# Kernel optimization log

Hardware: AMD Instinct MI355X
Metric: run time of the kernel (lower is better)

The kernel has to match this reference:

```python
import jax, jax.numpy as jnp
import numpy as np

B, L, IN_DIM, D, H, NCONV = 64, 400, 500, 128, 8, 4
HD = D // H  # head dim = 16


def _conv1d(x, w, b, pad, groups=1):
    # x: [B, L, Cin], w: [k, Cin//groups, Cout]
    y = jax.lax.conv_general_dilated(
        x, w, window_strides=(1,), padding=[(pad, pad)],
        dimension_numbers=('NWC', 'WIO', 'NWC'), feature_group_count=groups)
    return y + b


def _layernorm(x, g, b, eps=1e-5):
    mu = jnp.mean(x, axis=-1, keepdims=True)
    var = jnp.mean(jnp.square(x - mu), axis=-1, keepdims=True)
    return (x - mu) * jax.lax.rsqrt(var + eps) * g + b


def _posenc(L, d):
    pos = jnp.arange(L, dtype=jnp.float32)[:, None]                 # [L,1]
    div = jnp.exp(jnp.arange(0, d, 2, dtype=jnp.float32) * (-jnp.log(10000.0) / d))
    ang = pos * div                                                 # [L, d/2]
    return jnp.stack([jnp.sin(ang), jnp.cos(ang)], axis=-1).reshape(L, d)


def setup_inputs() -> dict:
    key = jax.random.key(0)
    ks = jax.random.split(key, 24)
    s = lambda k, shape, scale: jax.random.normal(k, shape, dtype=jnp.float32) * scale
    inp = {
        'x': s(ks[0], (B, L, IN_DIM), 1.0),
        # init conv: k=5, 500 -> 128
        'w_init': s(ks[1], (5, IN_DIM, D), 0.02),
        'b_init': jnp.zeros((D,), jnp.float32),
        # 4 depthwise-separable conv layers (pre-LN, residual): depthwise k=7
        'ln_conv_g': jnp.ones((NCONV, D), jnp.float32),
        'ln_conv_b': jnp.zeros((NCONV, D), jnp.float32),
        'w_dw': s(ks[2], (NCONV, 7, 1, D), 0.1),
        'b_dw': jnp.zeros((NCONV, D), jnp.float32),
        'w_pw': s(ks[3], (NCONV, 1, D, D), 0.05),
        'b_pw': jnp.zeros((NCONV, D), jnp.float32),
        # self-attention (pre-LN, residual)
        'ln_att_g': jnp.ones((D,), jnp.float32),
        'ln_att_b': jnp.zeros((D,), jnp.float32),
        'wq': s(ks[4], (D, D), 0.05), 'bq': jnp.zeros((D,), jnp.float32),
        'wk': s(ks[5], (D, D), 0.05), 'bk': jnp.zeros((D,), jnp.float32),
        'wv': s(ks[6], (D, D), 0.05), 'bv': jnp.zeros((D,), jnp.float32),
        'wo': s(ks[7], (D, D), 0.05), 'bo': jnp.zeros((D,), jnp.float32),
        # FFN (pre-LN, residual)
        'ln_ffn_g': jnp.ones((D,), jnp.float32),
        'ln_ffn_b': jnp.zeros((D,), jnp.float32),
        'w1': s(ks[8], (D, D), 0.05), 'b1': jnp.zeros((D,), jnp.float32),
        'w2': s(ks[9], (D, D), 0.05), 'b2': jnp.zeros((D,), jnp.float32),
    }
    return inp


def reference(x, w_init, b_init, ln_conv_g, ln_conv_b, w_dw, b_dw, w_pw, b_pw,
              ln_att_g, ln_att_b, wq, bq, wk, bk, wv, bv, wo, bo,
              ln_ffn_g, ln_ffn_b, w1, b1, w2, b2):
    # 1) init conv (Conv1d k=5 pad=2, 500 -> 128); torch permutes, equivalent NWC conv
    h = _conv1d(x, w_init, b_init, pad=2)                    # [B, L, D]
    # 2) positional encoding
    h = h + _posenc(h.shape[1], D)
    for i in range(NCONV):
        res = h
        h = _layernorm(h, ln_conv_g[i], ln_conv_b[i])
        h = _conv1d(h, w_dw[i], b_dw[i], pad=3, groups=D)    # depthwise k=7
        h = _conv1d(h, w_pw[i], b_pw[i], pad=0)              # pointwise 1x1
        h = jax.nn.relu(h) + res
    # 4) multi-head self-attention, pre-LN + residual
    res = h
    hn = _layernorm(h, ln_att_g, ln_att_b)
    q = (hn @ wq + bq).reshape(B, L, H, HD)
    k = (hn @ wk + bk).reshape(B, L, H, HD)
    v = (hn @ wv + bv).reshape(B, L, H, HD)
    scores = jnp.einsum('bqhd,bkhd->bhqk', q, k) / jnp.sqrt(jnp.float32(HD))
    attn = jax.nn.softmax(scores, axis=-1)
    o = jnp.einsum('bhqk,bkhd->bqhd', attn, v).reshape(B, L, D)
    h = o @ wo + bo + res
    # 5) FFN, pre-LN + residual
    res = h
    hn = _layernorm(h, ln_ffn_g, ln_ffn_b)
    h = jax.nn.relu(hn @ w1 + b1) @ w2 + b2 + res
    return h
```

## Files before the change

kernel.cpp:

```cpp
#include <hip/hip_runtime.h>
#include <hip/hip_bf16.h>
#include <math.h>

#define B 64
#define L 400
#define IN_DIM 500
#define D 128
#define H 8
#define HD 16
#define NCONV 4
#define BL (B*L)

typedef __attribute__((ext_vector_type(8))) unsigned short ushort8;
typedef __attribute__((ext_vector_type(8))) short bf16x8;
typedef __attribute__((ext_vector_type(4))) float f32x4;

__device__ __forceinline__ unsigned short f2bf(float f) {
    unsigned u = __float_as_uint(f);
    unsigned r = (u + 0x7fffu + ((u >> 16) & 1u)) >> 16;
    return (unsigned short)r;
}
__device__ __forceinline__ float bf2f(unsigned short u) {
    return __uint_as_float(((unsigned)u) << 16);
}
__device__ __forceinline__ unsigned cvtpk_bf16(float lo, float hi) {
    unsigned r;
    asm("v_cvt_pk_bf16_f32 %0, %1, %2" : "=v"(r) : "v"(lo), "v"(hi));
    return r;
}

__device__ __forceinline__ void gload16(const void* g, void* l) {
    __builtin_amdgcn_global_load_lds(
        (const __attribute__((address_space(1))) unsigned int*)g,
        (__attribute__((address_space(3))) unsigned int*)l,
        16, 0, 0);
}

__global__ __launch_bounds__(256) void k_cvt_all(
        const float* __restrict__ x, unsigned short* __restrict__ xb,
        const float* __restrict__ w_init, unsigned short* __restrict__ wbt,
        const float* __restrict__ w_pw, const float* __restrict__ wq,
        const float* __restrict__ wk, const float* __restrict__ wv,
        const float* __restrict__ wo, const float* __restrict__ w1,
        const float* __restrict__ w2, unsigned short* __restrict__ wt) {
    int bid = blockIdx.x;
    if (bid < 6464) {
        int idx = bid * 256 + threadIdx.x;
        int row = idx >> 6, ch = idx & 63;
        int b = row / 404, rr = row - b * 404;
        ushort8 o = (ushort8)0;
        if (rr >= 2 && rr < 402) {
            int l = rr - 2;
            const float* src = x + ((size_t)b * 400 + l) * 500 + ch * 8;
            if (ch < 62) {
                float4 v0 = *(const float4*)(src);
                float4 v1 = *(const float4*)(src + 4);
                o[0] = f2bf(v0.x); o[1] = f2bf(v0.y); o[2] = f2bf(v0.z); o[3] = f2bf(v0.w);
                o[4] = f2bf(v1.x); o[5] = f2bf(v1.y); o[6] = f2bf(v1.z); o[7] = f2bf(v1.w);
            } else {
#pragma unroll
                for (int j = 0; j < 8; ++j) {
                    int c = ch * 8 + j;
                    o[j] = (c < 500) ? f2bf(src[j]) : (unsigned short)0;
                }
            }
        }
        *(ushort8*)(xb + (size_t)idx * 8) = o;
    } else if (bid < 7744) {
        int idx = (bid - 6464) * 256 + threadIdx.x;
        int k = idx & 511, n = (idx >> 9) & 127, t = idx >> 16;
        float v = (k < 500) ? w_init[((size_t)t * 500 + k) * 128 + n] : 0.f;
        wbt[idx] = f2bf(v);
    } else {
        int rb = bid - 7744;
        const float* arr[10] = {w_pw, w_pw + 16384, w_pw + 2 * 16384,
                                w_pw + 3 * 16384, wq, wk, wv, wo, w1, w2};
        int widx = rb >> 6;
        const float* w = arr[widx];
        int idx = ((rb & 63) << 8) + threadIdx.x;
        int n = idx >> 7, k = idx & 127;
        wt[(size_t)widx * 16384 + idx] = f2bf(w[k * 128 + n]);
    }
}

#define TM 80
#define BK 64
__global__ __launch_bounds__(256) void k_initconv_mfma(
        const unsigned short* __restrict__ xb,
        const unsigned short* __restrict__ wbt,
        const float* __restrict__ bias, float* __restrict__ out) {
    __shared__ unsigned short As[84 * BK];
    __shared__ unsigned short Ws[5][64 * BK];
    int tid = threadIdx.x;
    int b = blockIdx.x / 10;
    int rem = blockIdx.x - b * 10;
    int l0 = (rem >> 1) * TM;
    int nh = rem & 1;
    int lane = tid & 63, wave = tid >> 6;
    int kgrp = lane >> 4, lm = lane & 15;

    f32x4 acc[5];
#pragma unroll
    for (int mf = 0; mf < 5; ++mf) acc[mf] = (f32x4)0.f;

    const unsigned short* abase = xb + ((size_t)(b * 404 + l0)) * 512;
    const unsigned short* wbase = wbt + (size_t)nh * 64 * 512;

    for (int k0 = 0; k0 < 512; k0 += BK) {
        for (int idx = tid; idx < 672; idx += 256) {
            int r = idx >> 3, sc = idx & 7;
            gload16(abase + (size_t)r * 512 + k0 + ((sc ^ (r & 7)) * 8),
                    As + idx * 8);
        }
#pragma unroll
        for (int i = 0; i < 10; ++i) {
            int idx = tid + i * 256;
            int t = idx >> 9;
            int sub = idx & 511;
            int n = sub >> 3, sc = sub & 7;
            gload16(wbase + (size_t)t * 128 * 512 + (size_t)n * 512 + k0
                        + ((sc ^ (n & 7)) * 8),
                    &Ws[t][0] + sub * 8);
        }
        __syncthreads();
        int n16 = wave * 16 + lm;
#pragma unroll
        for (int ks = 0; ks < 2; ++ks) {
            int gc = ks * 4 + kgrp;
            bf16x8 bfr[5];
#pragma unroll
            for (int t = 0; t < 5; ++t)
                bfr[t] = *(const bf16x8*)(&Ws[t][0] + n16 * 64
                                          + ((gc ^ (n16 & 7)) * 8));
#pragma unroll
            for (int mf = 0; mf < 5; ++mf) {
#pragma unroll
                for (int t = 0; t < 5; ++t) {
                    int r = mf * 16 + lm + t;
                    bf16x8 af = *(const bf16x8*)(As + r * 64
                                                 + ((gc ^ (r & 7)) * 8));
                    acc[mf] = __builtin_amdgcn_mfma_f32_16x16x32_bf16(
                        af, bfr[t], acc[mf], 0, 0, 0);
                }
            }
        }
        __syncthreads();
    }

    {
        int n = nh * 64 + wave * 16 + lm;
        float bs = bias[n];
        float pbase = expf(-(float)(n & ~1) * (9.210340371976184f / 128.0f));
#pragma unroll
        for (int mf = 0; mf < 5; ++mf) {
#pragma unroll
            for (int r = 0; r < 4; ++r) {
                int l = l0 + mf * 16 + kgrp * 4 + r;
                float ang = (float)l * pbase;
                float pe = (n & 1) ? cosf(ang) : sinf(ang);
                out[((size_t)b * 400 + l) * 128 + n] = acc[mf][r] + bs + pe;
            }
        }
    }
}

#define CB_ROWS 38
__global__ __launch_bounds__(256) void k_convblock(
        const float* __restrict__ hin, float* __restrict__ hout,
        const float* __restrict__ lng, const float* __restrict__ lnb,
        const float* __restrict__ wdw, const float* __restrict__ bdw,
        const unsigned short* __restrict__ wpt, const float* __restrict__ bpw) {
    __shared__ unsigned short Ws[128 * 128];
    __shared__ unsigned short Ln[CB_ROWS * 128];
    __shared__ unsigned short Dw[32 * 128];
    int tid = threadIdx.x;
    int b = blockIdx.x / 13;
    int tile = blockIdx.x - b * 13;
    int l0 = tile * 32;
    int lv = (l0 + 32 <= L) ? 32 : (L - l0);
    int lane = tid & 63, wave = tid >> 6;
    int lm = lane & 15, kgrp = lane >> 4;

#pragma unroll
    for (int i = 0; i < 8; ++i) {
        int idx = tid + i * 256;
        int n = idx >> 4, sc = idx & 15;
        gload16(wpt + (size_t)n * 128 + ((sc ^ (n & 15)) * 8), Ws + idx * 8);
    }

    {
        float2 gg = *(const float2*)(lng + lane * 2);
        float2 bb = *(const float2*)(lnb + lane * 2);
#pragma unroll
        for (int ri = 0; ri < 10; ++ri) {
            int r = wave + ri * 4;
            if (r < CB_ROWS) {
                int gl = l0 - 3 + r;
                bool ok = (gl >= 0 && gl < L);
                float2 v = make_float2(0.f, 0.f);
                if (ok) v = *(const float2*)(hin + ((size_t)b * L + gl) * 128 + lane * 2);
                float s = v.x + v.y;
                float q = v.x * v.x + v.y * v.y;
#pragma unroll
                for (int off = 32; off; off >>= 1) {
                    s += __shfl_xor(s, off);
                    q += __shfl_xor(q, off);
                }
                float mu  = s * (1.f / 128.f);
                float var = q * (1.f / 128.f) - mu * mu;
                float inv = rsqrtf(var + 1e-5f);
                unsigned pk = 0;
                if (ok) {
                    float ox = (v.x - mu) * inv * gg.x + bb.x;
                    float oy = (v.y - mu) * inv * gg.y + bb.y;
                    pk = (unsigned)f2bf(ox) | ((unsigned)f2bf(oy) << 16);
                }
                *(unsigned*)(Ln + r * 128 + lane * 2) = pk;
            }
        }
    }
    __syncthreads();

    {
        int d = tid & 127, half = tid >> 7;
        float wr[7];
#pragma unroll
        for (int t = 0; t < 7; ++t) wr[t] = wdw[t * 128 + d];
        float bs = bdw[d];
        float win[7];
#pragma unroll
        for (int t = 0; t < 6; ++t) win[t] = bf2f(Ln[(half * 16 + t) * 128 + d]);
#pragma unroll
        for (int lj = 0; lj < 16; ++lj) {
            int l = half * 16 + lj;
            win[6] = bf2f(Ln[(l + 6) * 128 + d]);
            float a = bs;
#pragma unroll
            for (int t = 0; t < 7; ++t) a = fmaf(win[t], wr[t], a);
#pragma unroll
            for (int t = 0; t < 6; ++t) win[t] = win[t + 1];
            Dw[l * 128 + ((d >> 3) ^ (l & 15)) * 8 + (d & 7)] = f2bf(a);
        }
    }
    __syncthreads();

    f32x4 acc[2][2];
#pragma unroll
    for (int mf = 0; mf < 2; ++mf)
#pragma unroll
        for (int nt = 0; nt < 2; ++nt) acc[mf][nt] = (f32x4)0.f;
#pragma unroll
    for (int kc = 0; kc < 4; ++kc) {
        int c = kc * 4 + kgrp;
        bf16x8 af[2];
#pragma unroll
        for (int mf = 0; mf < 2; ++mf) {
            int r = mf * 16 + lm;
            af[mf] = *(const bf16x8*)(Dw + r * 128 + (c ^ (r & 15)) * 8);
        }
#pragma unroll
        for (int nt = 0; nt < 2; ++nt) {
            int n = wave * 32 + nt * 16 + lm;
            bf16x8 bfv = *(const bf16x8*)(Ws + n * 128 + (c ^ (n & 15)) * 8);
#pragma unroll
            for (int mf = 0; mf < 2; ++mf)
                acc[mf][nt] = __builtin_amdgcn_mfma_f32_16x16x32_bf16(
                    af[mf], bfv, acc[mf][nt], 0, 0, 0);
        }
    }

#pragma unroll
    for (int nt = 0; nt < 2; ++nt) {
        int n = wave * 32 + nt * 16 + lm;
        float bsn = bpw[n];
#pragma unroll
        for (int mf = 0; mf < 2; ++mf) {
#pragma unroll
            for (int r = 0; r < 4; ++r) {
                int row = mf * 16 + kgrp * 4 + r;
                if (row < lv) {
                    size_t gi = ((size_t)b * L + l0 + row) * 128 + n;
                    hout[gi] = fmaxf(acc[mf][nt][r] + bsn, 0.f) + hin[gi];
                }
            }
        }
    }
}

__global__ __launch_bounds__(256) void k_ln_gemm(
        const float* __restrict__ h, const float* __restrict__ g,
        const float* __restrict__ bta, const unsigned short* __restrict__ wt0,
        int nw, const float* __restrict__ bias0, const float* __restrict__ bias1,
        const float* __restrict__ bias2, unsigned short* __restrict__ out0,
        unsigned short* __restrict__ out1, unsigned short* __restrict__ out2,
        float s0, int relu) {
    __shared__ unsigned short As[32 * 128];
    __shared__ unsigned short Ws[128 * 128];
    int tid = threadIdx.x;
    int m0 = blockIdx.x * 32;
    int lane = tid & 63, wave = tid >> 6;
    int lm = lane & 15, kgrp = lane >> 4;
    int wm = wave >> 1, wn = wave & 1;

#pragma unroll
    for (int i = 0; i < 8; ++i) {
        int idx = tid + i * 256;
        int n = idx >> 4, sc = idx & 15;
        gload16(wt0 + (size_t)n * 128 + ((sc ^ (n & 15)) * 8), Ws + idx * 8);
    }

    {
        float2 gg = *(const float2*)(g + lane * 2);
        float2 bb = *(const float2*)(bta + lane * 2);
#pragma unroll
        for (int ri = 0; ri < 8; ++ri) {
            int r = wave + ri * 4;
            float2 v = *(const float2*)(h + ((size_t)m0 + r) * 128 + lane * 2);
            float s = v.x + v.y;
            float q = v.x * v.x + v.y * v.y;
#pragma unroll
            for (int off = 32; off; off >>= 1) {
                s += __shfl_xor(s, off);
                q += __shfl_xor(q, off);
            }
            float mu  = s * (1.f / 128.f);
            float var = q * (1.f / 128.f) - mu * mu;
            float inv = rsqrtf(var + 1e-5f);
            float ox = (v.x - mu) * inv * gg.x + bb.x;
            float oy = (v.y - mu) * inv * gg.y + bb.y;
            unsigned pk = (unsigned)f2bf(ox) | ((unsigned)f2bf(oy) << 16);
            *(unsigned*)(As + r * 128 + ((lane >> 2) ^ (r & 15)) * 8
                         + ((lane * 2) & 7)) = pk;
        }
    }

    for (int i = 0; i < nw; ++i) {
        __syncthreads();
        f32x4 acc[4];
#pragma unroll
        for (int nt = 0; nt < 4; ++nt) acc[nt] = (f32x4)0.f;
#pragma unroll
        for (int kc = 0; kc < 4; ++kc) {
            int c = kc * 4 + kgrp;
            int r = wm * 16 + lm;
            bf16x8 af = *(const bf16x8*)(As + r * 128 + (c ^ (r & 15)) * 8);
#pragma unroll
            for (int nt = 0; nt < 4; ++nt) {
                int n = wn * 64 + nt * 16 + lm;
                bf16x8 bfv = *(const bf16x8*)(Ws + n * 128 + (c ^ (n & 15)) * 8);
                acc[nt] = __builtin_amdgcn_mfma_f32_16x16x32_bf16(
                    af, bfv, acc[nt], 0, 0, 0);
            }
        }
        const float* bias = (i == 0) ? bias0 : (i == 1) ? bias1 : bias2;
        unsigned short* out = (i == 0) ? out0 : (i == 1) ? out1 : out2;
        float sc0 = (i == 0) ? s0 : 1.f;
#pragma unroll
        for (int nt = 0; nt < 4; ++nt) {
            int n = wn * 64 + nt * 16 + lm;
            float bsn = bias[n];
#pragma unroll
            for (int r = 0; r < 4; ++r) {
                size_t m = (size_t)m0 + wm * 16 + kgrp * 4 + r;
                float v = acc[nt][r] + bsn;
                if (relu) v = fmaxf(v, 0.f);
                out[m * 128 + n] = f2bf(v * sc0);
            }
        }
        if (i + 1 < nw) {
            __syncthreads();
            const unsigned short* wp = wt0 + (size_t)(i + 1) * 16384;
#pragma unroll
            for (int j = 0; j < 8; ++j) {
                int idx = tid + j * 256;
                int n = idx >> 4, sc = idx & 15;
                gload16(wp + (size_t)n * 128 + ((sc ^ (n & 15)) * 8), Ws + idx * 8);
            }
        }
    }
}

__global__ __launch_bounds__(256) void k_gemm_bf16(
        const unsigned short* __restrict__ A,
        const unsigned short* __restrict__ Wt,
        const float* __restrict__ bias,
        const float* __restrict__ res,
        float* __restrict__ outf,
        unsigned short* __restrict__ outb,
        int relu, float oscale) {
    __shared__ unsigned short As[32 * 128];
    __shared__ unsigned short Ws[128 * 128];
    int tid = threadIdx.x;
    int m0 = blockIdx.x * 32;
    int lane = tid & 63, wave = tid >> 6;
    int lm = lane & 15, kgrp = lane >> 4;
    int wm = wave >> 1, wn = wave & 1;

#pragma unroll
    for (int i = 0; i < 2; ++i) {
        int idx = tid + i * 256;
        int r = idx >> 4, sc = idx & 15;
        gload16(A + ((size_t)(m0 + r)) * 128 + ((sc ^ (r & 15)) * 8), As + idx * 8);
    }
#pragma unroll
    for (int i = 0; i < 8; ++i) {
        int idx = tid + i * 256;
        int n = idx >> 4, sc = idx & 15;
        gload16(Wt + ((size_t)n) * 128 + ((sc ^ (n & 15)) * 8), Ws + idx * 8);
    }
    __syncthreads();

    f32x4 acc[4];
#pragma unroll
    for (int nt = 0; nt < 4; ++nt) acc[nt] = (f32x4)0.f;

#pragma unroll
    for (int kc = 0; kc < 4; ++kc) {
        int c = kc * 4 + kgrp;
        int r = wm * 16 + lm;
        bf16x8 af = *(const bf16x8*)(As + (r * 16 + (c ^ (r & 15))) * 8);
#pragma unroll
        for (int nt = 0; nt < 4; ++nt) {
            int n = wn * 64 + nt * 16 + lm;
            bf16x8 bfv = *(const bf16x8*)(Ws + (n * 16 + (c ^ (n & 15))) * 8);
            acc[nt] = __builtin_amdgcn_mfma_f32_16x16x32_bf16(af, bfv, acc[nt], 0, 0, 0);
        }
    }

#pragma unroll
    for (int nt = 0; nt < 4; ++nt) {
        int n = wn * 64 + nt * 16 + lm;
        float bs = bias[n];
#pragma unroll
        for (int r = 0; r < 4; ++r) {
            size_t m = (size_t)m0 + wm * 16 + kgrp * 4 + r;
            float v = acc[nt][r] + bs;
            if (relu) v = fmaxf(v, 0.f);
            if (res)  v += res[m * 128 + n];
            if (outf) outf[m * 128 + n] = v;
            else      outb[m * 128 + n] = f2bf(v * oscale);
        }
    }
}

#define KS 40
#define VS 424
__global__ __launch_bounds__(512) void k_attn_mfma(
        const unsigned short* __restrict__ qb,
        const unsigned short* __restrict__ kb,
        const unsigned short* __restrict__ vb,
        unsigned short* __restrict__ out) {
    __shared__ __align__(16) unsigned short Kpad[400 * KS];
    __shared__ __align__(16) unsigned short Vt[16 * VS];
    __shared__ __align__(16) unsigned short Ptmp[8][16 * KS];
    int tid = threadIdx.x;
    int b = blockIdx.x & 63, h = blockIdx.x >> 6;
    int lane = tid & 63, wave = tid >> 6;
    int lm = lane & 15, g = lane >> 4;

    for (int idx = tid; idx < 800; idx += 512) {
        int l = idx >> 1, half = idx & 1;
        ushort8 kv = *(const ushort8*)(kb + ((size_t)(b * 400 + l)) * 128 + h * 16 + half * 8);
        *(ushort8*)(Kpad + l * KS + half * 8) = kv;
        *(ushort8*)(Kpad + l * KS + 16 + half * 8) = (ushort8)0;
    }
    for (int idx = tid; idx < 800; idx += 512) {
        int kk = idx >> 1, dh = idx & 1;
        ushort8 vv = *(const ushort8*)(vb + ((size_t)(b * 400 + kk)) * 128 + h * 16 + dh * 8);
#pragma unroll
        for (int j = 0; j < 8; ++j) Vt[(dh * 8 + j) * VS + kk] = vv[j];
    }
    if (tid < 256) {
        int d = tid >> 4, kk = 400 + (tid & 15);
        Vt[d * VS + kk] = 0;
    }
    __syncthreads();

    unsigned short* Pw = Ptmp[wave];
    for (int tt = wave; tt < 25; tt += 8) {
        int q0 = tt * 16;
        bf16x8 Qf = *(const bf16x8*)(qb + ((size_t)(b * 400 + q0 + lm)) * 128 + h * 16 + g * 8);
        f32x4 s[25];
        __builtin_amdgcn_s_setprio(1);
#pragma unroll
        for (int kt = 0; kt < 25; ++kt) {
            bf16x8 Kf = *(const bf16x8*)(Kpad + (kt * 16 + lm) * KS + g * 8);
            s[kt] = __builtin_amdgcn_mfma_f32_16x16x32_bf16(Kf, Qf, (f32x4)0.f, 0, 0, 0);
        }
        __builtin_amdgcn_s_setprio(0);
        float m = -1e30f;
#pragma unroll
        for (int kt = 0; kt < 25; ++kt)
            m = fmaxf(m, fmaxf(fmaxf(s[kt][0], s[kt][1]),
                               fmaxf(s[kt][2], s[kt][3])));
        m = fmaxf(m, __shfl_xor(m, 16));
        m = fmaxf(m, __shfl_xor(m, 32));

        f32x4 O = (f32x4)0.f;
        f32x4 sumv = (f32x4)0.f;
#pragma unroll
        for (int kc = 0; kc < 13; ++kc) {
            {
                int kt = 2 * kc;
                f32x4 p;
                p[0] = __expf(s[kt][0] - m);
                p[1] = __expf(s[kt][1] - m);
                p[2] = __expf(s[kt][2] - m);
                p[3] = __expf(s[kt][3] - m);
                sumv += p;
                uint2 w; w.x = cvtpk_bf16(p[0], p[1]); w.y = cvtpk_bf16(p[2], p[3]);
                *(uint2*)(Pw + lm * KS + g * 4) = w;
            }
            {
                int kt = 2 * kc + 1;
                uint2 w; w.x = 0u; w.y = 0u;
                if (kt < 25) {
                    f32x4 p;
                    p[0] = __expf(s[kt][0] - m);
                    p[1] = __expf(s[kt][1] - m);
                    p[2] = __expf(s[kt][2] - m);
                    p[3] = __expf(s[kt][3] - m);
                    sumv += p;
                    w.x = cvtpk_bf16(p[0], p[1]); w.y = cvtpk_bf16(p[2], p[3]);
                }
                *(uint2*)(Pw + lm * KS + 16 + g * 4) = w;
            }
            __builtin_amdgcn_wave_barrier();
            asm volatile("s_waitcnt lgkmcnt(0)" ::: "memory");
            __builtin_amdgcn_sched_barrier(0);
            bf16x8 Pf = *(const bf16x8*)(Pw + lm * KS + g * 8);
            bf16x8 Vf = *(const bf16x8*)(Vt + lm * VS + kc * 32 + g * 8);
            O = __builtin_amdgcn_mfma_f32_16x16x32_bf16(Pf, Vf, O, 0, 0, 0);
            __builtin_amdgcn_wave_barrier();
        }
        float sum = (sumv[0] + sumv[1]) + (sumv[2] + sumv[3]);
        sum += __shfl_xor(sum, 16);
        sum += __shfl_xor(sum, 32);
        float rinv = 1.f / sum;
#pragma unroll
        for (int r = 0; r < 4; ++r) {
            float rq = __shfl(rinv, g * 4 + r);
            int q = q0 + g * 4 + r;
            out[((size_t)(b * 400 + q)) * 128 + h * 16 + lm] = f2bf(O[r] * rq);
        }
    }
}

extern "C" void kernel_launch(void* const* d_in, const int* in_sizes, int n_in,
                              void* d_out, int out_size, void* d_ws, size_t ws_size,
                              hipStream_t stream) {
    (void)in_sizes; (void)n_in; (void)out_size; (void)ws_size;
    const float* x      = (const float*)d_in[0];
    const float* w_init = (const float*)d_in[1];
    const float* b_init = (const float*)d_in[2];
    const float* lncg   = (const float*)d_in[3];
    const float* lncb   = (const float*)d_in[4];
    const float* w_dw   = (const float*)d_in[5];
    const float* b_dw   = (const float*)d_in[6];
    const float* w_pw   = (const float*)d_in[7];
    const float* b_pw   = (const float*)d_in[8];
    const float* lnag   = (const float*)d_in[9];
    const float* lnab   = (const float*)d_in[10];
    const float* wq     = (const float*)d_in[11];
    const float* bq     = (const float*)d_in[12];
    const float* wk     = (const float*)d_in[13];
    const float* bk     = (const float*)d_in[14];
    const float* wv     = (const float*)d_in[15];
    const float* bv     = (const float*)d_in[16];
    const float* wo     = (const float*)d_in[17];
    const float* bo     = (const float*)d_in[18];
    const float* lnfg   = (const float*)d_in[19];
    const float* lnfb   = (const float*)d_in[20];
    const float* w1     = (const float*)d_in[21];
    const float* b1     = (const float*)d_in[22];
    const float* w2     = (const float*)d_in[23];
    const float* b2     = (const float*)d_in[24];

    float* ws = (float*)d_ws;
    const size_t NBL = (size_t)BL * D;
    float* h0 = ws;
    float* outp = (float*)d_out;

    unsigned short* hnb = (unsigned short*)(ws + NBL);
    unsigned short* t0b = hnb + NBL;
    unsigned short* qb  = t0b + NBL;
    unsigned short* kb  = qb + NBL;
    unsigned short* vb  = kb + NBL;
    unsigned short* wt  = vb + NBL;
    unsigned short* xb  = wt + 10 * 16384;
    unsigned short* wbt = xb + (size_t)64 * 404 * 512;
    float* h1 = (float*)(wbt + (size_t)5 * 128 * 512);

    k_cvt_all<<<8384, 256, 0, stream>>>(x, xb, w_init, wbt,
                                        w_pw, wq, wk, wv, wo, w1, w2, wt);

    k_initconv_mfma<<<640, 256, 0, stream>>>(xb, wbt, b_init, h0);

    for (int i = 0; i < NCONV; ++i) {
        const float* hin = (i & 1) ? h1 : h0;
        float* hout      = (i & 1) ? h0 : h1;
        k_convblock<<<832, 256, 0, stream>>>(
            hin, hout, lncg + i * D, lncb + i * D,
            w_dw + (size_t)i * 7 * D, b_dw + i * D,
            wt + (size_t)i * 16384, b_pw + i * D);
    }

    k_ln_gemm<<<800, 256, 0, stream>>>(h0, lnag, lnab, wt + 4 * 16384, 3,
                                       bq, bk, bv, qb, kb, vb, 0.25f, 0);
    k_attn_mfma<<<512, 512, 0, stream>>>(qb, kb, vb, t0b);
    k_gemm_bf16<<<800, 256, 0, stream>>>(t0b, wt + 7 * 16384, bo, h0,
                                         h0, nullptr, 0, 1.f);

    k_ln_gemm<<<800, 256, 0, stream>>>(h0, lnfg, lnfb, wt + 8 * 16384, 1,
                                       b1, nullptr, nullptr,
                                       t0b, nullptr, nullptr, 1.f, 1);
    k_gemm_bf16<<<800, 256, 0, stream>>>(t0b, wt + 9 * 16384, b2, h0,
                                         outp, nullptr, 0, 1.f);
}
```

Baseline: 321.8 us.

## Fuse output projection, FFN layernorm, and both FFN GEMMs into one kernel

Replaces three launches (o-proj GEMM, LN+W1 GEMM, W2 GEMM) with one kernel per 32-row tile. The residual stream and the ReLU intermediate stay in shared memory, which removes the global round-trips of h0 and the bf16 intermediate and saves two launches. The cost is sequential loading of three weight matrices per block with no overlap, and higher LDS use (about 64KB), which may lower occupancy.

```diff
diff --git a/kernel.cpp b/kernel.cpp
--- a/kernel.cpp
+++ b/kernel.cpp
@@ -380,16 +380,18 @@
     }
 }
 
-__global__ __launch_bounds__(256) void k_gemm_bf16(
+__global__ __launch_bounds__(256) void k_oproj_ffn(
         const unsigned short* __restrict__ A,
-        const unsigned short* __restrict__ Wt,
-        const float* __restrict__ bias,
         const float* __restrict__ res,
-        float* __restrict__ outf,
-        unsigned short* __restrict__ outb,
-        int relu, float oscale) {
+        const unsigned short* __restrict__ wot, const float* __restrict__ bo,
+        const float* __restrict__ lng, const float* __restrict__ lnb,
+        const unsigned short* __restrict__ w1t, const float* __restrict__ b1,
+        const unsigned short* __restrict__ w2t, const float* __restrict__ b2,
+        float* __restrict__ outp) {
+    __shared__ unsigned short Ws[128 * 128];
     __shared__ unsigned short As[32 * 128];
-    __shared__ unsigned short Ws[128 * 128];
+    __shared__ float Hm[32 * 128];
+    __shared__ unsigned short Mid[32 * 128];
     int tid = threadIdx.x;
     int m0 = blockIdx.x * 32;
     int lane = tid & 63, wave = tid >> 6;
@@ -397,48 +399,145 @@
     int wm = wave >> 1, wn = wave & 1;
 
 #pragma unroll
+    for (int i = 0; i < 8; ++i) {
+        int idx = tid + i * 256;
+        int n = idx >> 4, sc = idx & 15;
+        gload16(wot + (size_t)n * 128 + ((sc ^ (n & 15)) * 8), Ws + idx * 8);
+    }
+#pragma unroll
     for (int i = 0; i < 2; ++i) {
         int idx = tid + i * 256;
         int r = idx >> 4, sc = idx & 15;
         gload16(A + ((size_t)(m0 + r)) * 128 + ((sc ^ (r & 15)) * 8), As + idx * 8);
     }
+    __syncthreads();
+
+    {
+        f32x4 acc[4];
+#pragma unroll
+        for (int nt = 0; nt < 4; ++nt) acc[nt] = (f32x4)0.f;
+#pragma unroll
+        for (int kc = 0; kc < 4; ++kc) {
+            int c = kc * 4 + kgrp;
+            int r = wm * 16 + lm;
+            bf16x8 af = *(const bf16x8*)(As + (r * 16 + (c ^ (r & 15))) * 8);
+#pragma unroll
+            for (int nt = 0; nt < 4; ++nt) {
+                int n = wn * 64 + nt * 16 + lm;
+                bf16x8 bfv = *(const bf16x8*)(Ws + (n * 16 + (c ^ (n & 15))) * 8);
+                acc[nt] = __builtin_amdgcn_mfma_f32_16x16x32_bf16(af, bfv, acc[nt], 0, 0, 0);
+            }
+        }
+#pragma unroll
+        for (int nt = 0; nt < 4; ++nt) {
+            int n = wn * 64 + nt * 16 + lm;
+            float bsn = bo[n];
+#pragma unroll
+            for (int r = 0; r < 4; ++r) {
+                int row = wm * 16 + kgrp * 4 + r;
+                Hm[row * 128 + n] = acc[nt][r] + bsn
+                                    + res[((size_t)m0 + row) * 128 + n];
+            }
+        }
+    }
+    __syncthreads();
+
 #pragma unroll
     for (int i = 0; i < 8; ++i) {
         int idx = tid + i * 256;
         int n = idx >> 4, sc = idx & 15;
-        gload16(Wt + ((size_t)n) * 128 + ((sc ^ (n & 15)) * 8), Ws + idx * 8);
+        gload16(w1t + (size_t)n * 128 + ((sc ^ (n & 15)) * 8), Ws + idx * 8);
+    }
+    {
+        float2 gg = *(const float2*)(lng + lane * 2);
+        float2 bb = *(const float2*)(lnb + lane * 2);
+#pragma unroll
+        for (int ri = 0; ri < 8; ++ri) {
+            int r = wave + ri * 4;
+            float2 v = *(const float2*)(Hm + r * 128 + lane * 2);
+            float s = v.x + v.y;
+            float q = v.x * v.x + v.y * v.y;
+#pragma unroll
+            for (int off = 32; off; off >>= 1) {
+                s += __shfl_xor(s, off);
+                q += __shfl_xor(q, off);
+            }
+            float mu  = s * (1.f / 128.f);
+            float var = q * (1.f / 128.f) - mu * mu;
+            float inv = rsqrtf(var + 1e-5f);
+            float ox = (v.x - mu) * inv * gg.x + bb.x;
+            float oy = (v.y - mu) * inv * gg.y + bb.y;
+            unsigned pk = (unsigned)f2bf(ox) | ((unsigned)f2bf(oy) << 16);
+            *(unsigned*)(As + r * 128 + ((lane >> 2) ^ (r & 15)) * 8
+                         + ((lane * 2) & 7)) = pk;
+        }
     }
     __syncthreads();
 
-    f32x4 acc[4];
-#pragma unroll
-    for (int nt = 0; nt < 4; ++nt) acc[nt] = (f32x4)0.f;
-
-#pragma unroll
-    for (int kc = 0; kc < 4; ++kc) {
-        int c = kc * 4 + kgrp;
-        int r = wm * 16 + lm;
-        bf16x8 af = *(const bf16x8*)(As + (r * 16 + (c ^ (r & 15))) * 8);
+    {
+        f32x4 acc[4];
+#pragma unroll
+        for (int nt = 0; nt < 4; ++nt) acc[nt] = (f32x4)0.f;
+#pragma unroll
+        for (int kc = 0; kc < 4; ++kc) {
+            int c = kc * 4 + kgrp;
+            int r = wm * 16 + lm;
+            bf16x8 af = *(const bf16x8*)(As + (r * 16 + (c ^ (r & 15))) * 8);
+#pragma unroll
+            for (int nt = 0; nt < 4; ++nt) {
+                int n = wn * 64 + nt * 16 + lm;
+                bf16x8 bfv = *(const bf16x8*)(Ws + (n * 16 + (c ^ (n & 15))) * 8);
+                acc[nt] = __builtin_amdgcn_mfma_f32_16x16x32_bf16(af, bfv, acc[nt], 0, 0, 0);
+            }
+        }
 #pragma unroll
         for (int nt = 0; nt < 4; ++nt) {
             int n = wn * 64 + nt * 16 + lm;
-            bf16x8 bfv = *(const bf16x8*)(Ws + (n * 16 + (c ^ (n & 15))) * 8);
-            acc[nt] = __builtin_amdgcn_mfma_f32_16x16x32_bf16(af, bfv, acc[nt], 0, 0, 0);
-        }
-    }
-
-#pragma unroll
-    for (int nt = 0; nt < 4; ++nt) {
-        int n = wn * 64 + nt * 16 + lm;
-        float bs = bias[n];
-#pragma unroll
-        for (int r = 0; r < 4; ++r) {
-            size_t m = (size_t)m0 + wm * 16 + kgrp * 4 + r;
-            float v = acc[nt][r] + bs;
-            if (relu) v = fmaxf(v, 0.f);
-            if (res)  v += res[m * 128 + n];
-            if (outf) outf[m * 128 + n] = v;
-            else      outb[m * 128 + n] = f2bf(v * oscale);
+            float bsn = b1[n];
+#pragma unroll
+            for (int r = 0; r < 4; ++r) {
+                int row = wm * 16 + kgrp * 4 + r;
+                float v = fmaxf(acc[nt][r] + bsn, 0.f);
+                Mid[row * 128 + ((n >> 3) ^ (row & 15)) * 8 + (n & 7)] = f2bf(v);
+            }
+        }
+    }
+    __syncthreads();
+
+#pragma unroll
+    for (int i = 0; i < 8; ++i) {
+        int idx = tid + i * 256;
+        int n = idx >> 4, sc = idx & 15;
+        gload16(w2t + (size_t)n * 128 + ((sc ^ (n & 15)) * 8), Ws + idx * 8);
+    }
+    __syncthreads();
+
+    {
+        f32x4 acc[4];
+#pragma unroll
+        for (int nt = 0; nt < 4; ++nt) acc[nt] = (f32x4)0.f;
+#pragma unroll
+        for (int kc = 0; kc < 4; ++kc) {
+            int c = kc * 4 + kgrp;
+            int r = wm * 16 + lm;
+            bf16x8 af = *(const bf16x8*)(Mid + (r * 16 + (c ^ (r & 15))) * 8);
+#pragma unroll
+            for (int nt = 0; nt < 4; ++nt) {
+                int n = wn * 64 + nt * 16 + lm;
+                bf16x8 bfv = *(const bf16x8*)(Ws + (n * 16 + (c ^ (n & 15))) * 8);
+                acc[nt] = __builtin_amdgcn_mfma_f32_16x16x32_bf16(af, bfv, acc[nt], 0, 0, 0);
+            }
+        }
+#pragma unroll
+        for (int nt = 0; nt < 4; ++nt) {
+            int n = wn * 64 + nt * 16 + lm;
+            float bsn = b2[n];
+#pragma unroll
+            for (int r = 0; r < 4; ++r) {
+                int row = wm * 16 + kgrp * 4 + r;
+                outp[((size_t)m0 + row) * 128 + n] =
+                    acc[nt][r] + bsn + Hm[row * 128 + n];
+            }
         }
     }
 }
@@ -608,12 +707,8 @@
     k_ln_gemm<<<800, 256, 0, stream>>>(h0, lnag, lnab, wt + 4 * 16384, 3,
                                        bq, bk, bv, qb, kb, vb, 0.25f, 0);
     k_attn_mfma<<<512, 512, 0, stream>>>(qb, kb, vb, t0b);
-    k_gemm_bf16<<<800, 256, 0, stream>>>(t0b, wt + 7 * 16384, bo, h0,
-                                         h0, nullptr, 0, 1.f);
-
-    k_ln_gemm<<<800, 256, 0, stream>>>(h0, lnfg, lnfb, wt + 8 * 16384, 1,
-                                       b1, nullptr, nullptr,
-                                       t0b, nullptr, nullptr, 1.f, 1);
-    k_gemm_bf16<<<800, 256, 0, stream>>>(t0b, wt + 9 * 16384, b2, h0,
-                                         outp, nullptr, 0, 1.f);
-}
+
+    k_oproj_ffn<<<800, 256, 0, stream>>>(
+        t0b, h0, wt + 7 * 16384, bo, lnfg, lnfb,
+        wt + 8 * 16384, b1, wt + 9 * 16384, b2, outp);
+}
```

Result: faster. 308.1 us (-4.3%).
